# Performance work log

Measured on AMD Instinct MI355X. Metric: run time of the kernel, lower is better.

The kernel has to match this reference:

```python
import jax, jax.numpy as jnp
import numpy as np

DIM = 2048
N_HEADS = 32
N_KV_HEADS = 8
HEAD_DIM = DIM // N_HEADS
B, T = 2, 2048


def setup_inputs() -> dict:
    key = jax.random.key(0)
    ks = jax.random.split(key, 5)
    std = 0.02
    return {
        "x": jax.random.normal(ks[0], (B, T, DIM), dtype=jnp.float32),
        "wq": jax.random.normal(ks[1], (DIM, DIM), dtype=jnp.float32) * std,
        "wk": jax.random.normal(ks[2], (N_KV_HEADS * HEAD_DIM, DIM), dtype=jnp.float32) * std,
        "wv": jax.random.normal(ks[3], (N_KV_HEADS * HEAD_DIM, DIM), dtype=jnp.float32) * std,
        "wo": jax.random.normal(ks[4], (DIM, DIM), dtype=jnp.float32) * std,
    }


def _rope_tables(seq_len, head_dim, dtype):
    inv_freq = 1.0 / (10000.0 ** (jnp.arange(0, head_dim, 2, dtype=jnp.float32) / head_dim))
    t = jnp.arange(seq_len, dtype=jnp.float32)
    freqs = jnp.einsum("i,j->ij", t, inv_freq)          # [T, hd/2]
    emb = jnp.concatenate([freqs, freqs], axis=-1)       # [T, hd]
    return jnp.cos(emb).astype(dtype), jnp.sin(emb).astype(dtype)


def _rotate_half(x):
    h = x.shape[-1] // 2
    return jnp.concatenate([-x[..., h:], x[..., :h]], axis=-1)


def reference(x, wq, wk, wv, wo):
    Bc, Tc, C = x.shape
    q = (x @ wq.T).reshape(Bc, Tc, N_HEADS, HEAD_DIM).transpose(0, 2, 1, 3)      # [B,H,T,hd]
    k = (x @ wk.T).reshape(Bc, Tc, N_KV_HEADS, HEAD_DIM).transpose(0, 2, 1, 3)   # [B,Hk,T,hd]
    v = (x @ wv.T).reshape(Bc, Tc, N_KV_HEADS, HEAD_DIM).transpose(0, 2, 1, 3)

    cos, sin = _rope_tables(Tc, HEAD_DIM, x.dtype)  # [T,hd] broadcast over B,H
    q = q * cos + _rotate_half(q) * sin
    k = k * cos + _rotate_half(k) * sin

    rep = N_HEADS // N_KV_HEADS
    k = jnp.repeat(k, rep, axis=1)  # [B,H,T,hd]
    v = jnp.repeat(v, rep, axis=1)

    scale = 1.0 / np.sqrt(HEAD_DIM)
    scores = jnp.einsum("bhqd,bhkd->bhqk", q, k) * scale   # [B,H,T,T]
    causal = jnp.triu(jnp.ones((Tc, Tc), dtype=bool), k=1)
    scores = jnp.where(causal, jnp.asarray(-jnp.inf, scores.dtype), scores)
    attn = jax.nn.softmax(scores, axis=-1)
    out = jnp.einsum("bhqk,bhkd->bhqd", attn, v)           # [B,H,T,hd]
    out = out.transpose(0, 2, 1, 3).reshape(Bc, Tc, C)
    return out @ wo.T
```

## Files before the change

### kernel.cpp

```cpp
#include <hip/hip_runtime.h>


typedef unsigned short u16;
typedef __attribute__((ext_vector_type(8))) short bf16x8;
typedef __attribute__((ext_vector_type(4))) float f32x4;
typedef __attribute__((ext_vector_type(4))) unsigned short u16x4;

constexpr int T_SEQ = 2048;
constexpr int DIMC  = 2048;
constexpr int NHEAD = 32;
constexpr int HDIM  = 64;
constexpr int KVDIM = 512;
constexpr int BATCH = 2;

__device__ __forceinline__ u16 f2bf(float f) {
    union { float f; unsigned int i; } v; v.f = f;
    unsigned int r = v.i + 0x7FFFu + ((v.i >> 16) & 1u);
    return (u16)(r >> 16);
}

__device__ __forceinline__ unsigned int pack2_bf16(float e0, float e1) {
    return __builtin_amdgcn_perm(__float_as_uint(e1), __float_as_uint(e0),
                                 0x07060302u);
}

typedef __attribute__((address_space(1))) unsigned int as1_uint;
typedef __attribute__((address_space(3))) unsigned int as3_uint;
__device__ __forceinline__ void glds16(const u16* g, u16* l) {
    __builtin_amdgcn_global_load_lds((as1_uint*)(u16*)g, (as3_uint*)l, 16, 0, 0);
}

__global__ __launch_bounds__(256) void cvt5(const float* __restrict__ x,
                                            const float* __restrict__ wq,
                                            const float* __restrict__ wk,
                                            const float* __restrict__ wv,
                                            const float* __restrict__ wo,
                                            u16* __restrict__ xb,  u16* __restrict__ wqb,
                                            u16* __restrict__ wkb, u16* __restrict__ wvb,
                                            u16* __restrict__ wob) {
    constexpr int E0 = BATCH * T_SEQ * DIMC;
    constexpr int E1 = E0 + DIMC * DIMC;
    constexpr int E2 = E1 + KVDIM * DIMC;
    constexpr int E3 = E2 + KVDIM * DIMC;
    constexpr int E4 = E3 + DIMC * DIMC;
    for (int i = (blockIdx.x * 256 + threadIdx.x) * 4; i < E4; i += gridDim.x * 1024) {
        const float* s; u16* d; int off;
        if (i < E0)      { s = x;  d = xb;  off = 0;  }
        else if (i < E1) { s = wq; d = wqb; off = E0; }
        else if (i < E2) { s = wk; d = wkb; off = E1; }
        else if (i < E3) { s = wv; d = wvb; off = E2; }
        else             { s = wo; d = wob; off = E3; }
        f32x4 v = *(const f32x4*)(s + (i - off));
        u16x4 o;
        #pragma unroll
        for (int e = 0; e < 4; ++e) o[e] = f2bf(v[e]);
        *(u16x4*)(d + (i - off)) = o;
    }
}

template <bool OUTF32>
__device__ __forceinline__ void gemm_core(const u16* __restrict__ A,
                                          const u16* __restrict__ W,
                                          void* __restrict__ Cv,
                                          int rowBase, int colBase,
                                          int N, int K, bool rope) {
    __shared__ __align__(16) u16 As[2 * 128 * 32];
    __shared__ __align__(16) u16 Bs[2 * 128 * 32];

    const int tid  = threadIdx.x;
    const int lane = tid & 63;
    const int w    = tid >> 6;
    const int quad = lane >> 4;
    const int ln   = lane & 15;
    const int wm = (w >> 1) * 64;
    const int wn = (w & 1) * 64;

    f32x4 acc[4][4] = {};

    const int srow = lane >> 2;
    const int scol = (lane & 3) * 8;
    const u16* aC0 = A + (size_t)(rowBase + w * 16 + srow) * K + scol;
    const u16* aC1 = A + (size_t)(rowBase + (w + 4) * 16 + srow) * K + scol;
    const u16* bC0 = W + (size_t)(colBase + w * 16 + srow) * K + scol;
    const u16* bC1 = W + (size_t)(colBase + (w + 4) * 16 + srow) * K + scol;
    u16* asl0 = As + w * 512;
    u16* asl1 = As + (w + 4) * 512;
    u16* bsl0 = Bs + w * 512;
    u16* bsl1 = Bs + (w + 4) * 512;

    for (int kk = 0; kk < K; kk += 64) {
        __syncthreads();
        glds16(aC0 + kk, asl0);
        glds16(aC1 + kk, asl1);
        glds16(bC0 + kk, bsl0);
        glds16(bC1 + kk, bsl1);
        glds16(aC0 + kk + 32, asl0 + 4096);
        glds16(aC1 + kk + 32, asl1 + 4096);
        glds16(bC0 + kk + 32, bsl0 + 4096);
        glds16(bC1 + kk + 32, bsl1 + 4096);
        __syncthreads();

        #pragma unroll
        for (int hp = 0; hp < 2; ++hp) {
            const u16* Ap = As + hp * 4096;
            const u16* Bp = Bs + hp * 4096;
            bf16x8 bw[4];
            #pragma unroll
            for (int j = 0; j < 4; ++j)
                bw[j] = *(const bf16x8*)(Bp + (wn + j * 16 + ln) * 32 + quad * 8);
            #pragma unroll
            for (int i = 0; i < 4; ++i) {
                bf16x8 af = *(const bf16x8*)(Ap + (wm + i * 16 + ln) * 32 + quad * 8);
                #pragma unroll
                for (int j = 0; j < 4; ++j)
                    acc[i][j] = __builtin_amdgcn_mfma_f32_16x16x32_bf16(af, bw[j], acc[i][j], 0, 0, 0);
            }
        }
    }

    if (rope) {
        #pragma unroll
        for (int j = 0; j < 2; ++j) {
            const int d = j * 16 + ln;
            const float invrev = exp2f(-(float)d * (13.287712379549449f / 32.0f))
                                 * 0.15915494309189535f;
            #pragma unroll
            for (int i = 0; i < 4; ++i) {
                #pragma unroll
                for (int r = 0; r < 4; ++r) {
                    const int t = (rowBase + wm + i * 16 + quad * 4 + r) & (T_SEQ - 1);
                    float rev = (float)t * invrev;
                    float fr = rev - floorf(rev);
                    float sn = __builtin_amdgcn_sinf(fr);
                    float cs = __builtin_amdgcn_cosf(fr);
                    float a0 = acc[i][j][r], a2 = acc[i][j + 2][r];
                    acc[i][j][r]     = a0 * cs - a2 * sn;
                    acc[i][j + 2][r] = a2 * cs + a0 * sn;
                }
            }
        }
    }

    #pragma unroll
    for (int i = 0; i < 4; ++i) {
        int mrow = rowBase + wm + i * 16 + quad * 4;
        #pragma unroll
        for (int j = 0; j < 4; ++j) {
            int n = colBase + wn + j * 16 + ln;
            #pragma unroll
            for (int r = 0; r < 4; ++r) {
                if constexpr (OUTF32)
                    ((float*)Cv)[(size_t)(mrow + r) * N + n] = acc[i][j][r];
                else
                    ((u16*)Cv)[(size_t)(mrow + r) * N + n] = f2bf(acc[i][j][r]);
            }
        }
    }
}

__global__ __launch_bounds__(256, 4) void qkv_gemm(const u16* __restrict__ xb,
                                                   const u16* __restrict__ wqb,
                                                   const u16* __restrict__ wkb,
                                                   const u16* __restrict__ wvb,
                                                   u16* __restrict__ Qb,
                                                   u16* __restrict__ Kb,
                                                   u16* __restrict__ Vb) {
    const int nb = blockIdx.x;
    const int rowBase = blockIdx.y * 128;
    const u16* W; u16* C; int colBase, N; bool rope;
    if (nb < 16)      { W = wqb; C = Qb; colBase = nb * 128;        N = DIMC;  rope = true; }
    else if (nb < 20) { W = wkb; C = Kb; colBase = (nb - 16) * 128; N = KVDIM; rope = true; }
    else              { W = wvb; C = Vb; colBase = (nb - 20) * 128; N = KVDIM; rope = false; }
    gemm_core<false>(xb, W, C, rowBase, colBase, N, DIMC, rope);
}

__global__ __launch_bounds__(256, 4) void gemm_out64(const u16* __restrict__ A,
                                                     const u16* __restrict__ W,
                                                     float* __restrict__ C) {
    __shared__ __align__(16) u16 As[2 * 128 * 32];
    __shared__ __align__(16) u16 Bs[2 * 64 * 32];

    const int tid  = threadIdx.x;
    const int lane = tid & 63;
    const int w    = tid >> 6;
    const int quad = lane >> 4;
    const int ln   = lane & 15;
    const int rowBase = blockIdx.y * 128;
    const int colBase = blockIdx.x * 64;
    const int wm = w * 32;
    constexpr int K = DIMC, N = DIMC;

    f32x4 acc[2][4] = {};

    const int srow = lane >> 2;
    const int scol = (lane & 3) * 8;
    const u16* aC0 = A + (size_t)(rowBase + w * 16 + srow) * K + scol;
    const u16* aC1 = A + (size_t)(rowBase + (w + 4) * 16 + srow) * K + scol;
    const u16* bC  = W + (size_t)(colBase + w * 16 + srow) * K + scol;
    u16* asl0 = As + w * 512;
    u16* asl1 = As + (w + 4) * 512;
    u16* bsl  = Bs + w * 512;

    for (int kk = 0; kk < K; kk += 64) {
        __syncthreads();
        glds16(aC0 + kk, asl0);
        glds16(aC1 + kk, asl1);
        glds16(bC  + kk, bsl);
        glds16(aC0 + kk + 32, asl0 + 4096);
        glds16(aC1 + kk + 32, asl1 + 4096);
        glds16(bC  + kk + 32, bsl + 2048);
        __syncthreads();

        #pragma unroll
        for (int hp = 0; hp < 2; ++hp) {
            const u16* Ap = As + hp * 4096;
            const u16* Bp = Bs + hp * 2048;
            bf16x8 bw[4];
            #pragma unroll
            for (int j = 0; j < 4; ++j)
                bw[j] = *(const bf16x8*)(Bp + (j * 16 + ln) * 32 + quad * 8);
            #pragma unroll
            for (int i = 0; i < 2; ++i) {
                bf16x8 af = *(const bf16x8*)(Ap + (wm + i * 16 + ln) * 32 + quad * 8);
                #pragma unroll
                for (int j = 0; j < 4; ++j)
                    acc[i][j] = __builtin_amdgcn_mfma_f32_16x16x32_bf16(af, bw[j], acc[i][j], 0, 0, 0);
            }
        }
    }

    #pragma unroll
    for (int i = 0; i < 2; ++i) {
        int mrow = rowBase + wm + i * 16 + quad * 4;
        #pragma unroll
        for (int j = 0; j < 4; ++j) {
            int n = colBase + j * 16 + ln;
            #pragma unroll
            for (int r = 0; r < 4; ++r)
                C[(size_t)(mrow + r) * N + n] = acc[i][j][r];
        }
    }
}

__global__ __launch_bounds__(256) void transpose_v(const u16* __restrict__ V,
                                                   u16* __restrict__ Vt) {
    __shared__ __align__(16) u16 tile[32][33];
    const int x = threadIdx.x & 31;
    const int y = threadIdx.x >> 5;
    const int tok0 = blockIdx.y * 32;
    const int c0   = blockIdx.x * 32;
    #pragma unroll
    for (int yy = 0; yy < 32; yy += 8)
        tile[y + yy][x] = V[(size_t)(tok0 + y + yy) * KVDIM + c0 + x];
    __syncthreads();
    const int b  = tok0 >> 11;
    const int t0 = tok0 & (T_SEQ - 1);
    #pragma unroll
    for (int yy = 0; yy < 32; yy += 8)
        Vt[(size_t)(b * KVDIM + c0 + y + yy) * T_SEQ + t0 + x] = tile[x][y + yy];
}

__global__ __launch_bounds__(256) void attn(const u16* __restrict__ Q,
                                            const u16* __restrict__ Kx,
                                            const u16* __restrict__ Vt,
                                            u16* __restrict__ O) {
    __shared__ __align__(16) u16 Ks[64][72];
    __shared__ __align__(16) u16 Vs[64][72];

    const int tid  = threadIdx.x;
    const int lane = tid & 63;
    const int w    = tid >> 6;
    const int quad = lane >> 4;
    const int ln   = lane & 15;
    const int h    = blockIdx.y;
    const int b    = blockIdx.z;
    const int kvh  = h >> 2;

    const int srow = tid >> 2;
    const int c    = tid & 3;
    const int scol = c * 16;
    const int vsb  = 32 * (c >> 1) + 4 * (c & 1);
    const u16* kbase = Kx + (size_t)(b * T_SEQ + srow) * KVDIM + kvh * HDIM + scol;
    const u16* vbase = Vt + (size_t)(b * KVDIM + kvh * HDIM + srow) * T_SEQ;

    const float K1 = 0.125f * 1.4426950408889634f;
    const float K2 = 8.0f * 1.4426950408889634f;

    #pragma unroll
    for (int phase = 0; phase < 2; ++phase) {
        const int qt = phase ? (31 - (int)blockIdx.x) : (int)blockIdx.x;
        const int qr0 = qt * 64 + w * 16;

        const u16* qp = Q + (size_t)(b * T_SEQ + qr0 + ln) * DIMC + h * HDIM + quad * 8;
        const bf16x8 bq0 = *(const bf16x8*)qp;
        const bf16x8 bq1 = *(const bf16x8*)(qp + 32);

        f32x4 o[4] = {};
        float lsum = 0.0f;

        bf16x8 kra = *(const bf16x8*)kbase;
        bf16x8 krb = *(const bf16x8*)(kbase + 8);
        bf16x8 vra = *(const bf16x8*)(vbase + scol);
        bf16x8 vrb = *(const bf16x8*)(vbase + scol + 8);

        for (int kt = 0; kt <= qt; ++kt) {
            __syncthreads();

            *(bf16x8*)&Ks[srow][scol]     = kra;
            *(bf16x8*)&Ks[srow][scol + 8] = krb;
            {
                union { bf16x8 v; u16x4 h4[2]; } ua, ub;
                ua.v = vra; ub.v = vrb;
                *(u16x4*)&Vs[srow][vsb]      = ua.h4[0];
                *(u16x4*)&Vs[srow][vsb + 8]  = ua.h4[1];
                *(u16x4*)&Vs[srow][vsb + 16] = ub.h4[0];
                *(u16x4*)&Vs[srow][vsb + 24] = ub.h4[1];
            }

            if (kt < qt) {
                const size_t ko = (size_t)(kt + 1) * 64;
                kra = *(const bf16x8*)(kbase + ko * KVDIM);
                krb = *(const bf16x8*)(kbase + ko * KVDIM + 8);
                vra = *(const bf16x8*)(vbase + ko + scol);
                vrb = *(const bf16x8*)(vbase + ko + scol + 8);
            }

            __asm__ __volatile__("s_waitcnt lgkmcnt(0)" ::: "memory");
            __builtin_amdgcn_s_barrier();

            f32x4 s[4];
            __builtin_amdgcn_s_setprio(1);
            #pragma unroll
            for (int st = 0; st < 4; ++st) {
                f32x4 z = {};
                s[st] = __builtin_amdgcn_mfma_f32_16x16x32_bf16(
                            *(const bf16x8*)&Ks[st * 16 + ln][quad * 8], bq0, z, 0, 0, 0);
                s[st] = __builtin_amdgcn_mfma_f32_16x16x32_bf16(
                            *(const bf16x8*)&Ks[st * 16 + ln][32 + quad * 8], bq1, s[st], 0, 0, 0);
            }
            __builtin_amdgcn_s_setprio(0);

            unsigned int pk[8];
            if (kt != qt) {
                #pragma unroll
                for (int st = 0; st < 4; ++st) {
                    float e0 = exp2f(fmaf(s[st][0], K1, -K2));
                    float e1 = exp2f(fmaf(s[st][1], K1, -K2));
                    float e2 = exp2f(fmaf(s[st][2], K1, -K2));
                    float e3 = exp2f(fmaf(s[st][3], K1, -K2));
                    lsum += (e0 + e1) + (e2 + e3);
                    pk[2 * st]     = pack2_bf16(e0, e1);
                    pk[2 * st + 1] = pack2_bf16(e2, e3);
                }
            } else {
                const int thr = w * 16 + ln;
                #pragma unroll
                for (int st = 0; st < 4; ++st) {
                    float e[4];
                    #pragma unroll
                    for (int r = 0; r < 4; ++r) {
                        const int key = st * 16 + quad * 4 + r;
                        e[r] = (key > thr) ? 0.0f : exp2f(fmaf(s[st][r], K1, -K2));
                    }
                    lsum += (e[0] + e[1]) + (e[2] + e[3]);
                    pk[2 * st]     = pack2_bf16(e[0], e[1]);
                    pk[2 * st + 1] = pack2_bf16(e[2], e[3]);
                }
            }

            union { unsigned int u[4]; bf16x8 v; } a0, a1;
            a0.u[0] = pk[0]; a0.u[1] = pk[1]; a0.u[2] = pk[2]; a0.u[3] = pk[3];
            a1.u[0] = pk[4]; a1.u[1] = pk[5]; a1.u[2] = pk[6]; a1.u[3] = pk[7];

            __builtin_amdgcn_s_setprio(1);
            #pragma unroll
            for (int t = 0; t < 4; ++t) {
                o[t] = __builtin_amdgcn_mfma_f32_16x16x32_bf16(
                           a0.v, *(const bf16x8*)&Vs[t * 16 + ln][quad * 8], o[t], 0, 0, 0);
                o[t] = __builtin_amdgcn_mfma_f32_16x16x32_bf16(
                           a1.v, *(const bf16x8*)&Vs[t * 16 + ln][32 + quad * 8], o[t], 0, 0, 0);
            }
            __builtin_amdgcn_s_setprio(0);
        }

        float ls = lsum;
        ls += __shfl_xor(ls, 16);
        ls += __shfl_xor(ls, 32);
        #pragma unroll
        for (int r = 0; r < 4; ++r) {
            const float inv = 1.0f / __shfl(ls, quad * 4 + r);
            size_t obase = (size_t)(b * T_SEQ + qr0 + quad * 4 + r) * DIMC + h * HDIM;
            #pragma unroll
            for (int t = 0; t < 4; ++t)
                O[obase + t * 16 + ln] = f2bf(o[t][r] * inv);
        }
    }
}

extern "C" void kernel_launch(void* const* d_in, const int* in_sizes, int n_in,
                              void* d_out, int out_size, void* d_ws, size_t ws_size,
                              hipStream_t stream) {
    const float* x  = (const float*)d_in[0];
    const float* wq = (const float*)d_in[1];
    const float* wk = (const float*)d_in[2];
    const float* wv = (const float*)d_in[3];
    const float* wo = (const float*)d_in[4];
    float* out = (float*)d_out;

    char* ws = (char*)d_ws;
    constexpr size_t MB = 1024 * 1024;
    u16* Qb  = (u16*)(ws);
    u16* Kb  = (u16*)(ws + 16 * MB);
    u16* Vb  = (u16*)(ws + 20 * MB);
    u16* Vtb = (u16*)(ws + 24 * MB);
    u16* AOb = (u16*)(ws + 28 * MB);
    u16* xb  = AOb;
    u16* wqb = (u16*)(ws + 44 * MB);
    u16* wkb = (u16*)(ws + 52 * MB);
    u16* wvb = (u16*)(ws + 54 * MB);
    u16* wob = (u16*)(ws + 56 * MB);
    const int M = BATCH * T_SEQ;

    hipLaunchKernelGGL(cvt5, dim3(2048), dim3(256), 0, stream,
                       x, wq, wk, wv, wo, xb, wqb, wkb, wvb, wob);
    hipLaunchKernelGGL(qkv_gemm, dim3(24, M / 128), dim3(256), 0, stream,
                       xb, wqb, wkb, wvb, Qb, Kb, Vb);
    hipLaunchKernelGGL(transpose_v, dim3(KVDIM / 32, M / 32), dim3(256), 0, stream, Vb, Vtb);
    hipLaunchKernelGGL(attn, dim3(16, NHEAD, BATCH), dim3(256), 0, stream,
                       Qb, Kb, Vtb, AOb);
    hipLaunchKernelGGL(gemm_out64, dim3(DIMC / 64, M / 128), dim3(256), 0, stream,
                       AOb, wob, out);
}
```

Measured before the change: 304.5 us.

## Rewrite QKV GEMM with 256x256 tiles, swizzled double-buffered LDS, and XCD-aware block remap

Replaces the 128x128 QKV projection GEMM with a 512-thread kernel computing 256x256 tiles. K-tiles of 64 go into XOR-swizzled, double-buffered shared memory, and the next tile's prefetch is interleaved with the MFMA work. Block indices are remapped so neighbouring tiles land on the same XCD, and the output GEMM gets the same remapping. The larger tiles give more data reuse per load and remove one sync per step, at the cost of 128KB of LDS and heavy register use, which limits occupancy.

```diff
diff --git a/kernel.cpp b/kernel.cpp
--- a/kernel.cpp
+++ b/kernel.cpp
@@ -58,135 +58,155 @@
     }
 }
 
-template <bool OUTF32>
-__device__ __forceinline__ void gemm_core(const u16* __restrict__ A,
-                                          const u16* __restrict__ W,
-                                          void* __restrict__ Cv,
-                                          int rowBase, int colBase,
-                                          int N, int K, bool rope) {
+__global__ __launch_bounds__(512, 2) void qkv_gemm8(const u16* __restrict__ xb,
+                                                    const u16* __restrict__ wqb,
+                                                    const u16* __restrict__ wkb,
+                                                    const u16* __restrict__ wvb,
+                                                    u16* __restrict__ Qb,
+                                                    u16* __restrict__ Kb,
+                                                    u16* __restrict__ Vb) {
+    __shared__ __align__(16) u16 Ash[2][256 * 64];
+    __shared__ __align__(16) u16 Bsh[2][256 * 64];
+
+    const int flat = blockIdx.y * 12 + blockIdx.x;
+    const int nf   = (flat & 7) * 24 + (flat >> 3);
+    const int ct   = nf % 12;
+    const int rt   = nf / 12;
+    const int rowBase = rt * 256;
+
+    const u16* W; u16* C; int colBase, N; bool rope;
+    if (ct < 8)       { W = wqb; C = Qb; colBase = ct * 256;        N = DIMC;  rope = true; }
+    else if (ct < 10) { W = wkb; C = Kb; colBase = (ct - 8) * 256;  N = KVDIM; rope = true; }
+    else              { W = wvb; C = Vb; colBase = (ct - 10) * 256; N = KVDIM; rope = false; }
+
+    const int tid  = threadIdx.x;
+    const int lane = tid & 63;
+    const int wid  = tid >> 6;
+    const int quad = lane >> 4;
+    const int ln   = lane & 15;
+    const int wr   = wid >> 2;
+    const int wc   = wid & 3;
+
+    const int sr = lane >> 3;
+    const int sc = 8 * ((lane & 7) ^ sr);
+    const u16* aS = xb + (size_t)(rowBase + wid * 8 + sr) * DIMC + sc;
+    const u16* bS = W  + (size_t)(colBase + wid * 8 + sr) * DIMC + sc;
+
+    f32x4 acc[8][4] = {};
+    constexpr int NT = DIMC / 64;
+
+    #pragma unroll
+    for (int r = 0; r < 4; ++r) {
+        glds16(aS + (size_t)r * 64 * DIMC, &Ash[0][(wid + 8 * r) * 512]);
+        glds16(bS + (size_t)r * 64 * DIMC, &Bsh[0][(wid + 8 * r) * 512]);
+    }
+
+    for (int t = 0; t < NT; ++t) {
+        const int cb = t & 1;
+        __asm__ __volatile__("s_waitcnt vmcnt(0)" ::: "memory");
+        __builtin_amdgcn_sched_barrier(0);
+        __builtin_amdgcn_s_barrier();
+
+        const u16* Ap = &Ash[cb][0];
+        const u16* Bp = &Bsh[cb][0];
+        u16* An = &Ash[cb ^ 1][0];
+        u16* Bn = &Bsh[cb ^ 1][0];
+        const bool pf = (t + 1 < NT);
+        const size_t ko = (size_t)(t + 1) * 64;
+        const int swz = (ln & 7) * 8;
+
+        #pragma unroll
+        for (int q2 = 0; q2 < 2; ++q2) {
+            bf16x8 bwf[4];
+            #pragma unroll
+            for (int n = 0; n < 4; ++n) {
+                const int row = wc * 64 + n * 16 + ln;
+                bwf[n] = *(const bf16x8*)(Bp + row * 64 + ((q2 * 32 + quad * 8) ^ swz));
+            }
+            if (q2 == 0 && pf) {
+                #pragma unroll
+                for (int r = 0; r < 2; ++r) {
+                    glds16(aS + ko + (size_t)r * 64 * DIMC, An + (wid + 8 * r) * 512);
+                    glds16(bS + ko + (size_t)r * 64 * DIMC, Bn + (wid + 8 * r) * 512);
+                }
+                __builtin_amdgcn_sched_barrier(0);
+            }
+            #pragma unroll
+            for (int mh = 0; mh < 2; ++mh) {
+                __builtin_amdgcn_s_setprio(1);
+                #pragma unroll
+                for (int m = mh * 4; m < mh * 4 + 4; ++m) {
+                    const int row = wr * 128 + m * 16 + ln;
+                    bf16x8 af = *(const bf16x8*)(Ap + row * 64 + ((q2 * 32 + quad * 8) ^ swz));
+                    #pragma unroll
+                    for (int n = 0; n < 4; ++n)
+                        acc[m][n] = __builtin_amdgcn_mfma_f32_16x16x32_bf16(af, bwf[n], acc[m][n], 0, 0, 0);
+                }
+                __builtin_amdgcn_s_setprio(0);
+                if (q2 == 0 && mh == 0 && pf) {
+                    #pragma unroll
+                    for (int r = 2; r < 4; ++r) {
+                        glds16(aS + ko + (size_t)r * 64 * DIMC, An + (wid + 8 * r) * 512);
+                        glds16(bS + ko + (size_t)r * 64 * DIMC, Bn + (wid + 8 * r) * 512);
+                    }
+                    __builtin_amdgcn_sched_barrier(0);
+                }
+            }
+        }
+    }
+
+    if (rope) {
+        #pragma unroll
+        for (int n = 0; n < 2; ++n) {
+            const int d = n * 16 + ln;
+            const float invrev = exp2f(-(float)d * (13.287712379549449f / 32.0f))
+                                 * 0.15915494309189535f;
+            #pragma unroll
+            for (int m = 0; m < 8; ++m) {
+                #pragma unroll
+                for (int r = 0; r < 4; ++r) {
+                    const int tt = (rowBase + wr * 128 + m * 16 + quad * 4 + r) & (T_SEQ - 1);
+                    float rev = (float)tt * invrev;
+                    float fr = rev - floorf(rev);
+                    float sn = __builtin_amdgcn_sinf(fr);
+                    float cs = __builtin_amdgcn_cosf(fr);
+                    float a0 = acc[m][n][r], a2 = acc[m][n + 2][r];
+                    acc[m][n][r]     = a0 * cs - a2 * sn;
+                    acc[m][n + 2][r] = a2 * cs + a0 * sn;
+                }
+            }
+        }
+    }
+
+    #pragma unroll
+    for (int m = 0; m < 8; ++m) {
+        const int mrow = rowBase + wr * 128 + m * 16 + quad * 4;
+        #pragma unroll
+        for (int n = 0; n < 4; ++n) {
+            const int col = colBase + wc * 64 + n * 16 + ln;
+            #pragma unroll
+            for (int r = 0; r < 4; ++r)
+                C[(size_t)(mrow + r) * N + col] = f2bf(acc[m][n][r]);
+        }
+    }
+}
+
+__global__ __launch_bounds__(256, 4) void gemm_out64(const u16* __restrict__ A,
+                                                     const u16* __restrict__ W,
+                                                     float* __restrict__ C) {
     __shared__ __align__(16) u16 As[2 * 128 * 32];
-    __shared__ __align__(16) u16 Bs[2 * 128 * 32];
+    __shared__ __align__(16) u16 Bs[2 * 64 * 32];
 
     const int tid  = threadIdx.x;
     const int lane = tid & 63;
     const int w    = tid >> 6;
     const int quad = lane >> 4;
     const int ln   = lane & 15;
-    const int wm = (w >> 1) * 64;
-    const int wn = (w & 1) * 64;
-
-    f32x4 acc[4][4] = {};
-
-    const int srow = lane >> 2;
-    const int scol = (lane & 3) * 8;
-    const u16* aC0 = A + (size_t)(rowBase + w * 16 + srow) * K + scol;
-    const u16* aC1 = A + (size_t)(rowBase + (w + 4) * 16 + srow) * K + scol;
-    const u16* bC0 = W + (size_t)(colBase + w * 16 + srow) * K + scol;
-    const u16* bC1 = W + (size_t)(colBase + (w + 4) * 16 + srow) * K + scol;
-    u16* asl0 = As + w * 512;
-    u16* asl1 = As + (w + 4) * 512;
-    u16* bsl0 = Bs + w * 512;
-    u16* bsl1 = Bs + (w + 4) * 512;
-
-    for (int kk = 0; kk < K; kk += 64) {
-        __syncthreads();
-        glds16(aC0 + kk, asl0);
-        glds16(aC1 + kk, asl1);
-        glds16(bC0 + kk, bsl0);
-        glds16(bC1 + kk, bsl1);
-        glds16(aC0 + kk + 32, asl0 + 4096);
-        glds16(aC1 + kk + 32, asl1 + 4096);
-        glds16(bC0 + kk + 32, bsl0 + 4096);
-        glds16(bC1 + kk + 32, bsl1 + 4096);
-        __syncthreads();
-
-        #pragma unroll
-        for (int hp = 0; hp < 2; ++hp) {
-            const u16* Ap = As + hp * 4096;
-            const u16* Bp = Bs + hp * 4096;
-            bf16x8 bw[4];
-            #pragma unroll
-            for (int j = 0; j < 4; ++j)
-                bw[j] = *(const bf16x8*)(Bp + (wn + j * 16 + ln) * 32 + quad * 8);
-            #pragma unroll
-            for (int i = 0; i < 4; ++i) {
-                bf16x8 af = *(const bf16x8*)(Ap + (wm + i * 16 + ln) * 32 + quad * 8);
-                #pragma unroll
-                for (int j = 0; j < 4; ++j)
-                    acc[i][j] = __builtin_amdgcn_mfma_f32_16x16x32_bf16(af, bw[j], acc[i][j], 0, 0, 0);
-            }
-        }
-    }
-
-    if (rope) {
-        #pragma unroll
-        for (int j = 0; j < 2; ++j) {
-            const int d = j * 16 + ln;
-            const float invrev = exp2f(-(float)d * (13.287712379549449f / 32.0f))
-                                 * 0.15915494309189535f;
-            #pragma unroll
-            for (int i = 0; i < 4; ++i) {
-                #pragma unroll
-                for (int r = 0; r < 4; ++r) {
-                    const int t = (rowBase + wm + i * 16 + quad * 4 + r) & (T_SEQ - 1);
-                    float rev = (float)t * invrev;
-                    float fr = rev - floorf(rev);
-                    float sn = __builtin_amdgcn_sinf(fr);
-                    float cs = __builtin_amdgcn_cosf(fr);
-                    float a0 = acc[i][j][r], a2 = acc[i][j + 2][r];
-                    acc[i][j][r]     = a0 * cs - a2 * sn;
-                    acc[i][j + 2][r] = a2 * cs + a0 * sn;
-                }
-            }
-        }
-    }
-
-    #pragma unroll
-    for (int i = 0; i < 4; ++i) {
-        int mrow = rowBase + wm + i * 16 + quad * 4;
-        #pragma unroll
-        for (int j = 0; j < 4; ++j) {
-            int n = colBase + wn + j * 16 + ln;
-            #pragma unroll
-            for (int r = 0; r < 4; ++r) {
-                if constexpr (OUTF32)
-                    ((float*)Cv)[(size_t)(mrow + r) * N + n] = acc[i][j][r];
-                else
-                    ((u16*)Cv)[(size_t)(mrow + r) * N + n] = f2bf(acc[i][j][r]);
-            }
-        }
-    }
-}
-
-__global__ __launch_bounds__(256, 4) void qkv_gemm(const u16* __restrict__ xb,
-                                                   const u16* __restrict__ wqb,
-                                                   const u16* __restrict__ wkb,
-                                                   const u16* __restrict__ wvb,
-                                                   u16* __restrict__ Qb,
-                                                   u16* __restrict__ Kb,
-                                                   u16* __restrict__ Vb) {
-    const int nb = blockIdx.x;
-    const int rowBase = blockIdx.y * 128;
-    const u16* W; u16* C; int colBase, N; bool rope;
-    if (nb < 16)      { W = wqb; C = Qb; colBase = nb * 128;        N = DIMC;  rope = true; }
-    else if (nb < 20) { W = wkb; C = Kb; colBase = (nb - 16) * 128; N = KVDIM; rope = true; }
-    else              { W = wvb; C = Vb; colBase = (nb - 20) * 128; N = KVDIM; rope = false; }
-    gemm_core<false>(xb, W, C, rowBase, colBase, N, DIMC, rope);
-}
-
-__global__ __launch_bounds__(256, 4) void gemm_out64(const u16* __restrict__ A,
-                                                     const u16* __restrict__ W,
-                                                     float* __restrict__ C) {
-    __shared__ __align__(16) u16 As[2 * 128 * 32];
-    __shared__ __align__(16) u16 Bs[2 * 64 * 32];
-
-    const int tid  = threadIdx.x;
-    const int lane = tid & 63;
-    const int w    = tid >> 6;
-    const int quad = lane >> 4;
-    const int ln   = lane & 15;
-    const int rowBase = blockIdx.y * 128;
-    const int colBase = blockIdx.x * 64;
+
+    const int flat = blockIdx.y * 32 + blockIdx.x;
+    const int nf   = (flat & 7) * 128 + (flat >> 3);
+    const int rowBase = (nf >> 5) * 128;
+    const int colBase = (nf & 31) * 64;
     const int wm = w * 32;
     constexpr int K = DIMC, N = DIMC;
 
@@ -423,7 +443,7 @@
 
     hipLaunchKernelGGL(cvt5, dim3(2048), dim3(256), 0, stream,
                        x, wq, wk, wv, wo, xb, wqb, wkb, wvb, wob);
-    hipLaunchKernelGGL(qkv_gemm, dim3(24, M / 128), dim3(256), 0, stream,
+    hipLaunchKernelGGL(qkv_gemm8, dim3(12, M / 256), dim3(512), 0, stream,
                        xb, wqb, wkb, wvb, Qb, Kb, Vb);
     hipLaunchKernelGGL(transpose_v, dim3(KVDIM / 32, M / 32), dim3(256), 0, stream, Vb, Vtb);
     hipLaunchKernelGGL(attn, dim3(16, NHEAD, BATCH), dim3(256), 0, stream,
```

Result: faster. 298.5 us (-2.0%).

## Double-buffer GEMM tiles with swizzled LDS and XCD-aware block remapping

Applied to the files above, without the earlier changes.

Replaces the GEMM core with a double-buffered pipeline: the next 64-wide K tile is prefetched into a second LDS buffer while MFMAs run on the current one, with one barrier per iteration instead of two. LDS rows use an XOR swizzle so fragment reads avoid bank conflicts. Block indices are remapped to spread tiles across XCDs, and setprio is raised around the MFMA loop. The output projection now reuses the same 128x128 core instead of a separate 128x64 kernel. This doubles LDS use and lowers the occupancy hint to 2 blocks per CU.

```diff
diff --git a/kernel.cpp b/kernel.cpp
--- a/kernel.cpp
+++ b/kernel.cpp
@@ -59,62 +59,74 @@
 }
 
 template <bool OUTF32>
-__device__ __forceinline__ void gemm_core(const u16* __restrict__ A,
-                                          const u16* __restrict__ W,
-                                          void* __restrict__ Cv,
-                                          int rowBase, int colBase,
-                                          int N, int K, bool rope) {
-    __shared__ __align__(16) u16 As[2 * 128 * 32];
-    __shared__ __align__(16) u16 Bs[2 * 128 * 32];
+__device__ __forceinline__ void dgemm_core(const u16* __restrict__ A,
+                                           const u16* __restrict__ W,
+                                           void* __restrict__ Cv,
+                                           int rowBase, int colBase,
+                                           int N, int K, bool rope) {
+    __shared__ __align__(16) u16 Ash[2][128 * 64];
+    __shared__ __align__(16) u16 Bsh[2][128 * 64];
 
     const int tid  = threadIdx.x;
     const int lane = tid & 63;
     const int w    = tid >> 6;
     const int quad = lane >> 4;
     const int ln   = lane & 15;
-    const int wm = (w >> 1) * 64;
-    const int wn = (w & 1) * 64;
+    const int wm   = (w >> 1) * 64;
+    const int wn   = (w & 1) * 64;
+
+    const int sr = lane >> 3;
+    const int sc = 8 * ((lane & 7) ^ sr);
+    const u16* aS = A + (size_t)(rowBase + w * 8 + sr) * K + sc;
+    const u16* bS = W + (size_t)(colBase + w * 8 + sr) * K + sc;
 
     f32x4 acc[4][4] = {};
-
-    const int srow = lane >> 2;
-    const int scol = (lane & 3) * 8;
-    const u16* aC0 = A + (size_t)(rowBase + w * 16 + srow) * K + scol;
-    const u16* aC1 = A + (size_t)(rowBase + (w + 4) * 16 + srow) * K + scol;
-    const u16* bC0 = W + (size_t)(colBase + w * 16 + srow) * K + scol;
-    const u16* bC1 = W + (size_t)(colBase + (w + 4) * 16 + srow) * K + scol;
-    u16* asl0 = As + w * 512;
-    u16* asl1 = As + (w + 4) * 512;
-    u16* bsl0 = Bs + w * 512;
-    u16* bsl1 = Bs + (w + 4) * 512;
-
-    for (int kk = 0; kk < K; kk += 64) {
-        __syncthreads();
-        glds16(aC0 + kk, asl0);
-        glds16(aC1 + kk, asl1);
-        glds16(bC0 + kk, bsl0);
-        glds16(bC1 + kk, bsl1);
-        glds16(aC0 + kk + 32, asl0 + 4096);
-        glds16(aC1 + kk + 32, asl1 + 4096);
-        glds16(bC0 + kk + 32, bsl0 + 4096);
-        glds16(bC1 + kk + 32, bsl1 + 4096);
-        __syncthreads();
-
-        #pragma unroll
-        for (int hp = 0; hp < 2; ++hp) {
-            const u16* Ap = As + hp * 4096;
-            const u16* Bp = Bs + hp * 4096;
-            bf16x8 bw[4];
-            #pragma unroll
-            for (int j = 0; j < 4; ++j)
-                bw[j] = *(const bf16x8*)(Bp + (wn + j * 16 + ln) * 32 + quad * 8);
-            #pragma unroll
-            for (int i = 0; i < 4; ++i) {
-                bf16x8 af = *(const bf16x8*)(Ap + (wm + i * 16 + ln) * 32 + quad * 8);
+    const int NT = K / 64;
+
+    #pragma unroll
+    for (int r = 0; r < 4; ++r) {
+        glds16(aS + (size_t)(r * 32) * K, &Ash[0][(w + 4 * r) * 512]);
+        glds16(bS + (size_t)(r * 32) * K, &Bsh[0][(w + 4 * r) * 512]);
+    }
+
+    for (int t = 0; t < NT; ++t) {
+        const int cb = t & 1;
+        __asm__ __volatile__("s_waitcnt vmcnt(0)" ::: "memory");
+        __builtin_amdgcn_sched_barrier(0);
+        __builtin_amdgcn_s_barrier();
+
+        if (t + 1 < NT) {
+            const size_t ko = (size_t)(t + 1) * 64;
+            u16* An = &Ash[cb ^ 1][0];
+            u16* Bn = &Bsh[cb ^ 1][0];
+            #pragma unroll
+            for (int r = 0; r < 4; ++r) {
+                glds16(aS + ko + (size_t)(r * 32) * K, An + (w + 4 * r) * 512);
+                glds16(bS + ko + (size_t)(r * 32) * K, Bn + (w + 4 * r) * 512);
+            }
+            __builtin_amdgcn_sched_barrier(0);
+        }
+
+        const u16* Ap = &Ash[cb][0];
+        const u16* Bp = &Bsh[cb][0];
+        const int swz = (ln & 7) * 8;
+        #pragma unroll
+        for (int q2 = 0; q2 < 2; ++q2) {
+            bf16x8 bwf[4];
+            #pragma unroll
+            for (int n = 0; n < 4; ++n)
+                bwf[n] = *(const bf16x8*)(Bp + (wn + n * 16 + ln) * 64
+                                             + ((q2 * 32 + quad * 8) ^ swz));
+            __builtin_amdgcn_s_setprio(1);
+            #pragma unroll
+            for (int m = 0; m < 4; ++m) {
+                bf16x8 af = *(const bf16x8*)(Ap + (wm + m * 16 + ln) * 64
+                                                + ((q2 * 32 + quad * 8) ^ swz));
                 #pragma unroll
-                for (int j = 0; j < 4; ++j)
-                    acc[i][j] = __builtin_amdgcn_mfma_f32_16x16x32_bf16(af, bw[j], acc[i][j], 0, 0, 0);
-            }
+                for (int n = 0; n < 4; ++n)
+                    acc[m][n] = __builtin_amdgcn_mfma_f32_16x16x32_bf16(af, bwf[n], acc[m][n], 0, 0, 0);
+            }
+            __builtin_amdgcn_s_setprio(0);
         }
     }
 
@@ -158,88 +170,33 @@
     }
 }
 
-__global__ __launch_bounds__(256, 4) void qkv_gemm(const u16* __restrict__ xb,
+__global__ __launch_bounds__(256, 2) void qkv_gemm(const u16* __restrict__ xb,
                                                    const u16* __restrict__ wqb,
                                                    const u16* __restrict__ wkb,
                                                    const u16* __restrict__ wvb,
                                                    u16* __restrict__ Qb,
                                                    u16* __restrict__ Kb,
                                                    u16* __restrict__ Vb) {
-    const int nb = blockIdx.x;
-    const int rowBase = blockIdx.y * 128;
+    const int flat = blockIdx.y * 24 + blockIdx.x;
+    const int nf   = (flat & 7) * 96 + (flat >> 3);
+    const int ct   = nf % 24;
+    const int rowBase = (nf / 24) * 128;
+
     const u16* W; u16* C; int colBase, N; bool rope;
-    if (nb < 16)      { W = wqb; C = Qb; colBase = nb * 128;        N = DIMC;  rope = true; }
-    else if (nb < 20) { W = wkb; C = Kb; colBase = (nb - 16) * 128; N = KVDIM; rope = true; }
-    else              { W = wvb; C = Vb; colBase = (nb - 20) * 128; N = KVDIM; rope = false; }
-    gemm_core<false>(xb, W, C, rowBase, colBase, N, DIMC, rope);
-}
-
-__global__ __launch_bounds__(256, 4) void gemm_out64(const u16* __restrict__ A,
-                                                     const u16* __restrict__ W,
-                                                     float* __restrict__ C) {
-    __shared__ __align__(16) u16 As[2 * 128 * 32];
-    __shared__ __align__(16) u16 Bs[2 * 64 * 32];
-
-    const int tid  = threadIdx.x;
-    const int lane = tid & 63;
-    const int w    = tid >> 6;
-    const int quad = lane >> 4;
-    const int ln   = lane & 15;
-    const int rowBase = blockIdx.y * 128;
-    const int colBase = blockIdx.x * 64;
-    const int wm = w * 32;
-    constexpr int K = DIMC, N = DIMC;
-
-    f32x4 acc[2][4] = {};
-
-    const int srow = lane >> 2;
-    const int scol = (lane & 3) * 8;
-    const u16* aC0 = A + (size_t)(rowBase + w * 16 + srow) * K + scol;
-    const u16* aC1 = A + (size_t)(rowBase + (w + 4) * 16 + srow) * K + scol;
-    const u16* bC  = W + (size_t)(colBase + w * 16 + srow) * K + scol;
-    u16* asl0 = As + w * 512;
-    u16* asl1 = As + (w + 4) * 512;
-    u16* bsl  = Bs + w * 512;
-
-    for (int kk = 0; kk < K; kk += 64) {
-        __syncthreads();
-        glds16(aC0 + kk, asl0);
-        glds16(aC1 + kk, asl1);
-        glds16(bC  + kk, bsl);
-        glds16(aC0 + kk + 32, asl0 + 4096);
-        glds16(aC1 + kk + 32, asl1 + 4096);
-        glds16(bC  + kk + 32, bsl + 2048);
-        __syncthreads();
-
-        #pragma unroll
-        for (int hp = 0; hp < 2; ++hp) {
-            const u16* Ap = As + hp * 4096;
-            const u16* Bp = Bs + hp * 2048;
-            bf16x8 bw[4];
-            #pragma unroll
-            for (int j = 0; j < 4; ++j)
-                bw[j] = *(const bf16x8*)(Bp + (j * 16 + ln) * 32 + quad * 8);
-            #pragma unroll
-            for (int i = 0; i < 2; ++i) {
-                bf16x8 af = *(const bf16x8*)(Ap + (wm + i * 16 + ln) * 32 + quad * 8);
-                #pragma unroll
-                for (int j = 0; j < 4; ++j)
-                    acc[i][j] = __builtin_amdgcn_mfma_f32_16x16x32_bf16(af, bw[j], acc[i][j], 0, 0, 0);
-            }
-        }
-    }
-
-    #pragma unroll
-    for (int i = 0; i < 2; ++i) {
-        int mrow = rowBase + wm + i * 16 + quad * 4;
-        #pragma unroll
-        for (int j = 0; j < 4; ++j) {
-            int n = colBase + j * 16 + ln;
-            #pragma unroll
-            for (int r = 0; r < 4; ++r)
-                C[(size_t)(mrow + r) * N + n] = acc[i][j][r];
-        }
-    }
+    if (ct < 16)      { W = wqb; C = Qb; colBase = ct * 128;        N = DIMC;  rope = true; }
+    else if (ct < 20) { W = wkb; C = Kb; colBase = (ct - 16) * 128; N = KVDIM; rope = true; }
+    else              { W = wvb; C = Vb; colBase = (ct - 20) * 128; N = KVDIM; rope = false; }
+    dgemm_core<false>(xb, W, C, rowBase, colBase, N, DIMC, rope);
+}
+
+__global__ __launch_bounds__(256, 2) void gemm_out(const u16* __restrict__ A,
+                                                   const u16* __restrict__ W,
+                                                   float* __restrict__ C) {
+    const int flat = blockIdx.y * 16 + blockIdx.x;
+    const int nf   = (flat & 7) * 64 + (flat >> 3);
+    const int colBase = (nf % 16) * 128;
+    const int rowBase = (nf / 16) * 128;
+    dgemm_core<true>(A, W, C, rowBase, colBase, DIMC, DIMC, false);
 }
 
 __global__ __launch_bounds__(256) void transpose_v(const u16* __restrict__ V,
@@ -428,6 +385,6 @@
     hipLaunchKernelGGL(transpose_v, dim3(KVDIM / 32, M / 32), dim3(256), 0, stream, Vb, Vtb);
     hipLaunchKernelGGL(attn, dim3(16, NHEAD, BATCH), dim3(256), 0, stream,
                        Qb, Kb, Vtb, AOb);
-    hipLaunchKernelGGL(gemm_out64, dim3(DIMC / 64, M / 128), dim3(256), 0, stream,
+    hipLaunchKernelGGL(gemm_out, dim3(DIMC / 128, M / 128), dim3(256), 0, stream,
                        AOb, wob, out);
 }
```

After: 297.3 us. 1.02x faster.
